# Optimization experiments

Measured on AMD Instinct MI355X. Metric: run time of the kernel, lower is better.

Reference implementation:

```python
import jax, jax.numpy as jnp
import numpy as np

NUM_CLASSES = 40
EOS_COEF = 0.1
IGNORE = 255
W_CLASS, W_MASK, W_DICE = 2.0, 5.0, 5.0
EPS = 1e-8


def setup_inputs() -> dict:
    key = jax.random.key(0)
    k1, k2, k3, k4 = jax.random.split(key, 4)
    B, Q, H, W = 4, 100, 256, 256
    pred_logits = jax.random.normal(k1, (B, Q, NUM_CLASSES + 1), dtype=jnp.float32)
    pred_masks = jax.random.normal(k2, (B, Q, H, W), dtype=jnp.float32)
    targets = jax.random.randint(k3, (B, H, W), 0, NUM_CLASSES)
    ign = jax.random.uniform(k4, (B, H, W)) < 0.05
    targets = jnp.where(ign, IGNORE, targets).astype(jnp.int32)
    return {"pred_logits": pred_logits, "pred_masks": pred_masks, "targets": targets}


def reference(pred_logits, pred_masks, targets):
    B, Q, _ = pred_logits.shape
    C = NUM_CLASSES
    f32 = jnp.float32
    valid = targets != IGNORE                      # [B,H,W]
    tgt_safe = jnp.where(valid, targets, 0)        # in-range for indexing

    # ---- loss_labels: pixel->query assignment, per-query mode label ----
    # sigmoid is monotone, so argmax over queries of raw logits == argmax of sigmoid
    assign = jnp.argmax(pred_masks, axis=1)        # [B,H,W]
    b_idx = jnp.broadcast_to(jnp.arange(B)[:, None, None], targets.shape)
    # counts[b,q,c] = #valid pixels assigned to query q with label c
    counts = jnp.zeros((B, Q, C), f32).at[b_idx, assign, tgt_safe].add(valid.astype(f32))
    has_pix = counts.sum(-1) > 0                   # [B,Q]
    # mode = argmax of counts (ties -> smallest class, matching torch.mode)
    target_classes = jnp.where(has_pix, jnp.argmax(counts, axis=-1), C)  # [B,Q]

    logp = jax.nn.log_softmax(pred_logits, axis=-1)                      # [B,Q,C+1]
    nll = -jnp.take_along_axis(logp, target_classes[..., None], axis=-1)[..., 0]
    empty_weight = jnp.ones(C + 1, f32).at[-1].set(EOS_COEF)
    # ignore_index = num_classes in the CE over classes
    ce = jnp.where(target_classes != C, nll * empty_weight[target_classes], 0.0)
    p = jnp.exp(-ce)
    loss_ce = jnp.mean((1.0 - p) ** 2 * ce)

    # ---- loss_masks: per-pixel CE over queries + per-class dice ----
    logp_pix = jax.nn.log_softmax(pred_masks, axis=1)                    # [B,Q,H,W]
    nll_pix = -jnp.take_along_axis(logp_pix, tgt_safe[:, None], axis=1)[:, 0]  # [B,H,W]
    n_valid = valid.astype(f32).sum()
    ce_mask = jnp.sum(jnp.where(valid, nll_pix, 0.0)) / jnp.maximum(n_valid, 1.0)

    sig = jax.nn.sigmoid(pred_masks)                                     # [B,Q,H,W]
    tmask = (targets[:, None] == jnp.arange(C)[None, :, None, None]).astype(f32)  # [B,C,H,W]
    vm = valid[:, None].astype(f32)                                      # [B,1,H,W]
    inter = jnp.einsum('bqhw,bchw->bqc', sig, tmask * vm)                # numerator uses valid mask
    src_sum = sig.sum(axis=(2, 3))                                       # [B,Q]
    tsum = tmask.sum(axis=(2, 3))                                        # [B,C]
    dice = 2.0 * inter / (src_sum[:, :, None] + tsum[:, None, :] + EPS)  # [B,Q,C]
    present = tsum.sum(axis=0) > 0                                       # [C]
    dice_loss = jnp.sum(jnp.where(present, 1.0 - dice.mean(axis=(0, 1)), 0.0)) / C

    combined = W_MASK * ce_mask + W_DICE * dice_loss
    return W_CLASS * loss_ce + combined
```

## Files before the change

### kernel.cpp

```cpp
#include <hip/hip_runtime.h>

constexpr int B = 4, Q = 100, C = 40, Cp1 = 41, HW = 65536;

constexpr int FBLKS = 512;

constexpr int WS_WORDS = 32562;

typedef __attribute__((ext_vector_type(8))) short short8;
typedef __attribute__((ext_vector_type(4))) float f32x4;

__device__ __forceinline__ short f2bf(float f) {
    unsigned u = __float_as_uint(f);
    u += 0x7FFF + ((u >> 16) & 1);
    return (short)(u >> 16);
}

__global__ void kZ(unsigned* __restrict__ ws, int n) {
    int i = blockIdx.x * blockDim.x + threadIdx.x;
    for (; i < n; i += gridDim.x * blockDim.x) ws[i] = 0u;
}

__global__ __launch_bounds__(256) void kF(const float* __restrict__ masks,
                                          const int* __restrict__ targets,
                                          unsigned* __restrict__ counts,
                                          unsigned* __restrict__ tsum,
                                          float* __restrict__ ce_sum,
                                          unsigned* __restrict__ n_valid,
                                          float* __restrict__ inter_ext) {
    __shared__ __align__(16) short tileS[16 * 512];
    __shared__ __align__(8) unsigned char tgt8[512];
    __shared__ float smem[160];

    const int tid = threadIdx.x;
    const int l = tid & 63, w = tid >> 6;
    const int m = l & 15, quad = l >> 4;

    const int blk = blockIdx.x;
    const int b = blk >> 7;
    const int seg = blk & 127;
    const int pxb = w * 128 + 2 * l;
    const int p0 = seg * 512 + pxb;

    const int2 tg = *(const int2*)(targets + (size_t)b * HW + p0);
    *(unsigned short*)&tgt8[pxb] =
        (unsigned short)((tg.x & 255) | ((tg.y & 255) << 8));
    unsigned* ts_local = (unsigned*)&smem[0];
    if (tid < C) ts_local[tid] = 0u;
    __syncthreads();

    const float* mp = masks + (size_t)b * Q * HW + p0;
    const int tg0 = tg.x, tg1 = tg.y;

    float m20 = -INFINITY, m21 = -INFINITY;
    float s0 = 0.f, s1 = 0.f, xt0 = 0.f, xt1 = 0.f;
    int am0 = 0, am1 = 0;

    char* tbytes = (char*)tileS;
    const int wbase = w * 256 + l * 4;

    const int colbase = w * 16;
    const int cv = (w == 2) ? ((m == 8) ? 255 : 32 + m) : (colbase + m);

    for (int qt = 0; qt < 7; ++qt) {
        const int nu = (qt == 6) ? 4 : 16;

        float2 vv[16];
        const float* mq = mp + (size_t)(qt * 16) * HW;
        #pragma unroll
        for (int u = 0; u < 16; ++u)
            if (u < nu) vv[u] = *(const float2*)(mq + (size_t)u * HW);

        #pragma unroll
        for (int u = 0; u < 16; ++u)
            if (u < nu) {
                const int q = qt * 16 + u;
                const float v0 = vv[u].x, v1 = vv[u].y;
                s0 += __expf(v0);
                s1 += __expf(v1);
                am0 = (v0 > m20) ? q : am0;  m20 = fmaxf(m20, v0);
                am1 = (v1 > m21) ? q : am1;  m21 = fmaxf(m21, v1);
                xt0 = (q == tg0) ? v0 : xt0;
                xt1 = (q == tg1) ? v1 : xt1;
                const float g0 = __builtin_amdgcn_rcpf(1.f + __expf(-v0));
                const float g1 = __builtin_amdgcn_rcpf(1.f + __expf(-v1));
                const unsigned pk = (unsigned)(unsigned short)f2bf(g0) |
                                    ((unsigned)(unsigned short)f2bf(g1) << 16);
                *(unsigned*)(tbytes + ((u * 1024 + wbase) ^ ((u & 7) << 4))) = pk;
            }

        asm volatile("s_waitcnt lgkmcnt(0)" ::: "memory");
        __builtin_amdgcn_s_barrier();
        asm volatile("" ::: "memory");

        f32x4 acc = {0.f, 0.f, 0.f, 0.f};
        if (w < 3) {
            #pragma unroll
            for (int kc = 0; kc < 16; ++kc) {
                const short8 av = *(const short8*)(tbytes +
                    ((m * 1024 + kc * 64 + quad * 16) ^ ((m & 7) << 4)));
                const unsigned long long tw =
                    *(const unsigned long long*)&tgt8[kc * 32 + quad * 8];
                short8 bv;
                #pragma unroll
                for (int j = 0; j < 8; ++j) {
                    const int tb = (int)((tw >> (8 * j)) & 255);
                    bv[j] = (tb == cv) ? (short)0x3F80 : (short)0;
                }
                acc = __builtin_amdgcn_mfma_f32_16x16x32_bf16(av, bv, acc, 0, 0, 0);
            }
        }
        asm volatile("" ::: "memory");
        __builtin_amdgcn_s_barrier();
        asm volatile("" ::: "memory");

        if (w < 3 && !(w == 2 && m > 8)) {
            #pragma unroll
            for (int reg = 0; reg < 4; ++reg) {
                const int q = qt * 16 + quad * 4 + reg;
                if (q < 100)
                    atomicAdd(&inter_ext[(size_t)(b * Q + q) * Cp1 + colbase + m],
                              acc[reg]);
            }
        }
    }

    float ce = 0.f;
    unsigned nv = 0u;
    if (tg0 != 255) {
        ce += __logf(s0) - xt0; nv++;
        atomicAdd(&counts[((size_t)b * Q + am0) * C + tg0], 1u);
        atomicAdd(&ts_local[tg0], 1u);
    }
    if (tg1 != 255) {
        ce += __logf(s1) - xt1; nv++;
        atomicAdd(&counts[((size_t)b * Q + am1) * C + tg1], 1u);
        atomicAdd(&ts_local[tg1], 1u);
    }
    for (int off = 32; off; off >>= 1) {
        ce += __shfl_xor(ce, off);
        nv += __shfl_xor(nv, off);
    }
    float* cred = &smem[64];
    unsigned* vred = (unsigned*)&smem[72];
    if (l == 0) { cred[w] = ce; vred[w] = nv; }
    __syncthreads();
    if (tid == 0) {
        atomicAdd(ce_sum, cred[0] + cred[1] + cred[2] + cred[3]);
        atomicAdd(n_valid, vred[0] + vred[1] + vred[2] + vred[3]);
    }
    if (tid < C) {
        unsigned t = ts_local[tid];
        if (t) atomicAdd(&tsum[b * C + tid], t);
    }
}

__global__ __launch_bounds__(512) void kC(const float* __restrict__ logits,
                                          const unsigned* __restrict__ counts,
                                          const unsigned* __restrict__ tsum,
                                          const float* __restrict__ inter_ext,
                                          const float* __restrict__ ce_sum,
                                          const unsigned* __restrict__ n_valid,
                                          float* __restrict__ out) {
    int tid = threadIdx.x;
    __shared__ float dice_sum[C];
    __shared__ float ssum[B * Q];
    __shared__ float wred[8];
    __shared__ float s_lce;
    if (tid < C) dice_sum[tid] = 0.f;
    if (tid < B * Q) {
        const float* r = inter_ext + (size_t)tid * Cp1;
        float t = 0.f;
        #pragma unroll
        for (int c = 0; c < Cp1; ++c) t += r[c];
        ssum[tid] = t;
    }

    float ce_acc = 0.f;
    for (int i = tid; i < B * Q; i += 512) {
        const unsigned* cnt = counts + (size_t)i * C;
        unsigned best = 0;
        int tc = C;
        #pragma unroll
        for (int c = 0; c < C; ++c) {
            unsigned v = cnt[c];
            if (v > best) { best = v; tc = c; }
        }
        if (tc != C) {
            const float* lg = logits + (size_t)i * Cp1;
            float mm = -INFINITY, xt = 0.f;
            #pragma unroll
            for (int c = 0; c < Cp1; ++c) {
                float v = lg[c];
                mm = fmaxf(mm, v);
                if (c == tc) xt = v;
            }
            float ss = 0.f;
            #pragma unroll
            for (int c = 0; c < Cp1; ++c) ss += __expf(lg[c] - mm);
            float nll = mm + __logf(ss) - xt;
            float p = __expf(-nll);
            float om = 1.f - p;
            ce_acc += om * om * nll;
        }
    }
    for (int off = 32; off; off >>= 1) ce_acc += __shfl_xor(ce_acc, off);
    if ((tid & 63) == 0) wred[tid >> 6] = ce_acc;
    __syncthreads();
    if (tid == 0) {
        float t = 0.f;
        for (int w = 0; w < 8; ++w) t += wred[w];
        s_lce = t;
    }

    for (int i = tid; i < B * Q * C; i += 512) {
        int bq = i / C, c = i - bq * C;
        float denom = ssum[bq] + (float)tsum[(bq / Q) * C + c] + 1e-8f;
        atomicAdd(&dice_sum[c], 2.f * inter_ext[(size_t)bq * Cp1 + c] / denom);
    }
    __syncthreads();

    if (tid == 0) {
        float dl = 0.f;
        for (int c = 0; c < C; ++c) {
            unsigned ts = tsum[c] + tsum[C + c] + tsum[2 * C + c] + tsum[3 * C + c];
            if (ts > 0) dl += 1.f - dice_sum[c] * (1.f / (B * Q));
        }
        dl *= (1.f / C);
        float ce_mask = ce_sum[0] / fmaxf((float)n_valid[0], 1.f);
        float lce = s_lce * (1.f / (B * Q));
        out[0] = 2.f * lce + 5.f * ce_mask + 5.f * dl;
    }
}

extern "C" void kernel_launch(void* const* d_in, const int* in_sizes, int n_in,
                              void* d_out, int out_size, void* d_ws, size_t ws_size,
                              hipStream_t stream) {
    const float* logits  = (const float*)d_in[0];
    const float* masks   = (const float*)d_in[1];
    const int*   targets = (const int*)d_in[2];
    float* out = (float*)d_out;

    unsigned* ws        = (unsigned*)d_ws;
    unsigned* counts    = ws;
    unsigned* tsum      = ws + 16000;
    float*    ce_sum    = (float*)(ws + 16160);
    unsigned* n_valid   = ws + 16161;
    float*    inter_ext = (float*)(ws + 16162);

    kZ<<<64, 256, 0, stream>>>(ws, WS_WORDS);
    kF<<<FBLKS, 256, 0, stream>>>(masks, targets, counts, tsum, ce_sum, n_valid,
                                  inter_ext);
    kC<<<1, 512, 0, stream>>>(logits, counts, tsum, inter_ext, ce_sum, n_valid, out);
}
```

Before: 220.7 us.

## Double-buffer LDS tile, accumulate intersections in shared memory, widen finalize block

Double-buffers the bf16 sigmoid tile so each query tile needs one barrier instead of two. The per-tile global float atomics on the intersection buffer become LDS atomics into a per-block 100x41 accumulator, which is flushed once at the end with nonzero-only global atomics. The finalize kernel also moves from 512 to 1024 threads. This raises LDS use per block (about 16KB more plus 32KB for the tiles), which may lower occupancy, and it adds an end-of-block flush.

```diff
diff --git a/kernel.cpp b/kernel.cpp
--- a/kernel.cpp
+++ b/kernel.cpp
@@ -27,9 +27,12 @@
                                           float* __restrict__ ce_sum,
                                           unsigned* __restrict__ n_valid,
                                           float* __restrict__ inter_ext) {
-    __shared__ __align__(16) short tileS[16 * 512];
+    __shared__ __align__(16) short tileS[2][16 * 512];
+    __shared__ float inter_lds[Q * Cp1];
     __shared__ __align__(8) unsigned char tgt8[512];
-    __shared__ float smem[160];
+    __shared__ unsigned ts_local[C];
+    __shared__ float cred[4];
+    __shared__ unsigned vred[4];
 
     const int tid = threadIdx.x;
     const int l = tid & 63, w = tid >> 6;
@@ -38,37 +41,35 @@
     const int blk = blockIdx.x;
     const int b = blk >> 7;
     const int seg = blk & 127;
-    const int pxb = w * 128 + 2 * l;
-    const int p0 = seg * 512 + pxb;
+    const int p0 = seg * 512 + 2 * tid;
 
     const int2 tg = *(const int2*)(targets + (size_t)b * HW + p0);
-    *(unsigned short*)&tgt8[pxb] =
-        (unsigned short)((tg.x & 255) | ((tg.y & 255) << 8));
-    unsigned* ts_local = (unsigned*)&smem[0];
+    const int tg0 = tg.x, tg1 = tg.y;
+    *(unsigned short*)&tgt8[2 * tid] =
+        (unsigned short)((tg0 & 255) | ((tg1 & 255) << 8));
     if (tid < C) ts_local[tid] = 0u;
-    __syncthreads();
+    #pragma unroll
+    for (int i = 0; i < 17; ++i) {
+        int idx = tid + i * 256;
+        if (idx < Q * Cp1) inter_lds[idx] = 0.f;
+    }
 
     const float* mp = masks + (size_t)b * Q * HW + p0;
-    const int tg0 = tg.x, tg1 = tg.y;
 
     float m20 = -INFINITY, m21 = -INFINITY;
     float s0 = 0.f, s1 = 0.f, xt0 = 0.f, xt1 = 0.f;
     int am0 = 0, am1 = 0;
 
-    char* tbytes = (char*)tileS;
-    const int wbase = w * 256 + l * 4;
-
-    const int colbase = w * 16;
-    const int cv = (w == 2) ? ((m == 8) ? 255 : 32 + m) : (colbase + m);
+    const int cv = (w == 2 && m == 8) ? 255 : (w * 16 + m);
 
     for (int qt = 0; qt < 7; ++qt) {
+        char* tbq = (char*)(&tileS[qt & 1][0]);
         const int nu = (qt == 6) ? 4 : 16;
 
         float2 vv[16];
-        const float* mq = mp + (size_t)(qt * 16) * HW;
         #pragma unroll
         for (int u = 0; u < 16; ++u)
-            if (u < nu) vv[u] = *(const float2*)(mq + (size_t)u * HW);
+            if (u < nu) vv[u] = *(const float2*)(mp + (size_t)(qt * 16 + u) * HW);
 
         #pragma unroll
         for (int u = 0; u < 16; ++u)
@@ -85,41 +86,34 @@
                 const float g1 = __builtin_amdgcn_rcpf(1.f + __expf(-v1));
                 const unsigned pk = (unsigned)(unsigned short)f2bf(g0) |
                                     ((unsigned)(unsigned short)f2bf(g1) << 16);
-                *(unsigned*)(tbytes + ((u * 1024 + wbase) ^ ((u & 7) << 4))) = pk;
-            }
-
-        asm volatile("s_waitcnt lgkmcnt(0)" ::: "memory");
-        __builtin_amdgcn_s_barrier();
-        asm volatile("" ::: "memory");
-
-        f32x4 acc = {0.f, 0.f, 0.f, 0.f};
+                *(unsigned*)(tbq + ((u * 1024 + 4 * tid) ^ ((u & 7) << 4))) = pk;
+            }
+
+        __syncthreads();
+
         if (w < 3) {
+            f32x4 acc = {0.f, 0.f, 0.f, 0.f};
             #pragma unroll
             for (int kc = 0; kc < 16; ++kc) {
-                const short8 av = *(const short8*)(tbytes +
+                const short8 av = *(const short8*)(tbq +
                     ((m * 1024 + kc * 64 + quad * 16) ^ ((m & 7) << 4)));
                 const unsigned long long tw =
                     *(const unsigned long long*)&tgt8[kc * 32 + quad * 8];
                 short8 bv;
                 #pragma unroll
-                for (int j = 0; j < 8; ++j) {
-                    const int tb = (int)((tw >> (8 * j)) & 255);
-                    bv[j] = (tb == cv) ? (short)0x3F80 : (short)0;
+                for (int j = 0; j < 8; ++j)
+                    bv[j] = ((int)((tw >> (8 * j)) & 255) == cv)
+                                ? (short)0x3F80 : (short)0;
+                acc = __builtin_amdgcn_mfma_f32_16x16x32_bf16(av, bv, acc,
+                                                              0, 0, 0);
+            }
+            if (!(w == 2 && m > 8)) {
+                #pragma unroll
+                for (int reg = 0; reg < 4; ++reg) {
+                    const int q = qt * 16 + quad * 4 + reg;
+                    if (q < 100)
+                        atomicAdd(&inter_lds[q * Cp1 + w * 16 + m], acc[reg]);
                 }
-                acc = __builtin_amdgcn_mfma_f32_16x16x32_bf16(av, bv, acc, 0, 0, 0);
-            }
-        }
-        asm volatile("" ::: "memory");
-        __builtin_amdgcn_s_barrier();
-        asm volatile("" ::: "memory");
-
-        if (w < 3 && !(w == 2 && m > 8)) {
-            #pragma unroll
-            for (int reg = 0; reg < 4; ++reg) {
-                const int q = qt * 16 + quad * 4 + reg;
-                if (q < 100)
-                    atomicAdd(&inter_ext[(size_t)(b * Q + q) * Cp1 + colbase + m],
-                              acc[reg]);
             }
         }
     }
@@ -140,8 +134,6 @@
         ce += __shfl_xor(ce, off);
         nv += __shfl_xor(nv, off);
     }
-    float* cred = &smem[64];
-    unsigned* vred = (unsigned*)&smem[72];
     if (l == 0) { cred[w] = ce; vred[w] = nv; }
     __syncthreads();
     if (tid == 0) {
@@ -152,19 +144,29 @@
         unsigned t = ts_local[tid];
         if (t) atomicAdd(&tsum[b * C + tid], t);
     }
-}
-
-__global__ __launch_bounds__(512) void kC(const float* __restrict__ logits,
-                                          const unsigned* __restrict__ counts,
-                                          const unsigned* __restrict__ tsum,
-                                          const float* __restrict__ inter_ext,
-                                          const float* __restrict__ ce_sum,
-                                          const unsigned* __restrict__ n_valid,
-                                          float* __restrict__ out) {
+
+    const size_t ibase = (size_t)b * Q * Cp1;
+    #pragma unroll
+    for (int i = 0; i < 17; ++i) {
+        int idx = tid + i * 256;
+        if (idx < Q * Cp1) {
+            float v = inter_lds[idx];
+            if (v != 0.f) atomicAdd(&inter_ext[ibase + idx], v);
+        }
+    }
+}
+
+__global__ __launch_bounds__(1024) void kC(const float* __restrict__ logits,
+                                           const unsigned* __restrict__ counts,
+                                           const unsigned* __restrict__ tsum,
+                                           const float* __restrict__ inter_ext,
+                                           const float* __restrict__ ce_sum,
+                                           const unsigned* __restrict__ n_valid,
+                                           float* __restrict__ out) {
     int tid = threadIdx.x;
     __shared__ float dice_sum[C];
     __shared__ float ssum[B * Q];
-    __shared__ float wred[8];
+    __shared__ float wred[16];
     __shared__ float s_lce;
     if (tid < C) dice_sum[tid] = 0.f;
     if (tid < B * Q) {
@@ -176,7 +178,7 @@
     }
 
     float ce_acc = 0.f;
-    for (int i = tid; i < B * Q; i += 512) {
+    for (int i = tid; i < B * Q; i += 1024) {
         const unsigned* cnt = counts + (size_t)i * C;
         unsigned best = 0;
         int tc = C;
@@ -208,11 +210,11 @@
     __syncthreads();
     if (tid == 0) {
         float t = 0.f;
-        for (int w = 0; w < 8; ++w) t += wred[w];
+        for (int w = 0; w < 16; ++w) t += wred[w];
         s_lce = t;
     }
 
-    for (int i = tid; i < B * Q * C; i += 512) {
+    for (int i = tid; i < B * Q * C; i += 1024) {
         int bq = i / C, c = i - bq * C;
         float denom = ssum[bq] + (float)tsum[(bq / Q) * C + c] + 1e-8f;
         atomicAdd(&dice_sum[c], 2.f * inter_ext[(size_t)bq * Cp1 + c] / denom);
@@ -250,5 +252,5 @@
     kZ<<<64, 256, 0, stream>>>(ws, WS_WORDS);
     kF<<<FBLKS, 256, 0, stream>>>(masks, targets, counts, tsum, ce_sum, n_valid,
                                   inter_ext);
-    kC<<<1, 512, 0, stream>>>(logits, counts, tsum, inter_ext, ce_sum, n_valid, out);
-}
+    kC<<<1, 1024, 0, stream>>>(logits, counts, tsum, inter_ext, ce_sum, n_valid, out);
+}
```

Measured after the change: 206.0 us. 6.6% less time.
